# Kernel tuning notes

Hardware: AMD Instinct MI355X
Metric: run time of the kernel (lower is better)

Reference implementation:

```python
import jax, jax.numpy as jnp
import numpy as np

N_NODES = 50000
N_EDGES = 800000
N_GRAPHS = 2048
F = 78  # num_features_xd


def gcn_conv(x, src, dst, W, b):
    """PyG GCNConv: x' = D^{-1/2}(A+I)D^{-1/2} (x W) + b, self-loops added."""
    n = x.shape[0]
    xw = x @ W  # dense transform first (PyG order)
    loop = jnp.arange(n)
    s = jnp.concatenate([src, loop])
    d = jnp.concatenate([dst, loop])
    deg = jax.ops.segment_sum(jnp.ones(d.shape[0], dtype=xw.dtype), d, num_segments=n)
    dis = jnp.where(deg > 0, jax.lax.rsqrt(deg), 0.0)
    norm = dis[s] * dis[d]  # [E+N]
    msg = xw[s] * norm[:, None]  # gather + scale, [E+N, Fout]
    out = jax.ops.segment_sum(msg, d, num_segments=n)  # scatter-add to targets
    return out + b


def setup_inputs() -> dict:
    key = jax.random.key(0)
    ks = jax.random.split(key, 9)

    def glorot(k, shape):
        lim = float(np.sqrt(6.0 / (shape[0] + shape[1])))
        return jax.random.uniform(k, shape, minval=-lim, maxval=lim, dtype=jnp.float32)

    x = jax.random.normal(ks[0], (N_NODES, F), dtype=jnp.float32)
    edge_index = jax.random.randint(ks[1], (2, N_EDGES), 0, N_NODES, dtype=jnp.int64)
    batch = jnp.sort(jax.random.randint(ks[2], (N_NODES,), 0, N_GRAPHS, dtype=jnp.int64))
    drug2 = jax.random.normal(ks[3], (N_GRAPHS, 489), dtype=jnp.float32)

    W1 = glorot(ks[4], (F, F));        b1 = jnp.zeros((F,), jnp.float32)
    W2 = glorot(ks[5], (F, 2 * F));    b2 = jnp.zeros((2 * F,), jnp.float32)
    W3 = glorot(ks[6], (2 * F, 4 * F)); b3 = jnp.zeros((4 * F,), jnp.float32)
    Wfc = glorot(ks[7], (4 * F, 489)); bfc = jnp.zeros((489,), jnp.float32)

    return dict(x=x, edge_index=edge_index, batch=batch, drug2=drug2,
                W1=W1, b1=b1, W2=W2, b2=b2, W3=W3, b3=b3, Wfc=Wfc, bfc=bfc)


def reference(x, edge_index, batch, drug2, W1, b1, W2, b2, W3, b3, Wfc, bfc):
    src, dst = edge_index[0], edge_index[1]
    h = jax.nn.relu(gcn_conv(x, src, dst, W1, b1))   # dropout = identity (eval mode)
    h = jax.nn.relu(gcn_conv(h, src, dst, W2, b2))
    h = jax.nn.relu(gcn_conv(h, src, dst, W3, b3))
    g = jax.ops.segment_max(h, batch, num_segments=N_GRAPHS)  # global max pool
    g = jnp.where(jnp.isfinite(g), g, 0.0)  # guard empty graphs
    g = jax.nn.relu(g @ Wfc + bfc)
    return g + drug2
```

## Files before the change

kernel.cpp:

```cpp
#include <hip/hip_runtime.h>

#define NNODES 50000
#define NEDGES 800000
#define NGRAPHS 2048

typedef __attribute__((ext_vector_type(8))) short bf16x8;
typedef __attribute__((ext_vector_type(4))) float f32x4;

__device__ __forceinline__ float bf2f(ushort u) {
    return __uint_as_float(((uint)u) << 16);
}
__device__ __forceinline__ ushort f2bf(float f) {
    uint u = __float_as_uint(f);
    return (ushort)((u + 0x7fff + ((u >> 16) & 1)) >> 16);
}

__global__ void deg_count(const int* __restrict__ dst, int* __restrict__ cnt, int E) {
    int e = blockIdx.x * blockDim.x + threadIdx.x;
    if (e < E) atomicAdd(&cnt[dst[e]], 1);
}

__global__ void block_scan(const int* __restrict__ cnt, int* __restrict__ lp,
                           int* __restrict__ bsum, int M) {
    __shared__ int s[256];
    int t = threadIdx.x;
    int n = blockIdx.x * 256 + t;
    int v = (n < M) ? cnt[n] : 0;
    s[t] = v;
    __syncthreads();
    #pragma unroll
    for (int off = 1; off < 256; off <<= 1) {
        int u = (t >= off) ? s[t - off] : 0;
        __syncthreads();
        s[t] += u;
        __syncthreads();
    }
    if (n < M) lp[n] = s[t] - v;
    if (t == 255) bsum[blockIdx.x] = s[255];
}

__global__ void scan_bsum(int* __restrict__ bsum, int NB) {
    __shared__ int s[256];
    int t = threadIdx.x;
    int v = (t < NB) ? bsum[t] : 0;
    s[t] = v;
    __syncthreads();
    #pragma unroll
    for (int off = 1; off < 256; off <<= 1) {
        int u = (t >= off) ? s[t - off] : 0;
        __syncthreads();
        s[t] += u;
        __syncthreads();
    }
    if (t < NB) bsum[t] = s[t] - v;
}

__global__ void finalize_rowptr(int* __restrict__ rowptr, int* __restrict__ cursor,
                                const int* __restrict__ bsum, const int* __restrict__ cnt,
                                float* __restrict__ dis, int M, int E) {
    int n = blockIdx.x * blockDim.x + threadIdx.x;
    if (n < M) {
        int v = rowptr[n] + bsum[n >> 8];
        rowptr[n] = v;
        cursor[n] = v;
        dis[n] = rsqrtf((float)(cnt[n] + 1));
    }
    if (n == 0) rowptr[M] = E;
}

__global__ void fill_csr(const int* __restrict__ src, const int* __restrict__ dst,
                         const float* __restrict__ dis, int* __restrict__ cursor,
                         int2* __restrict__ csr, int E) {
    int e = blockIdx.x * blockDim.x + threadIdx.x;
    if (e >= E) return;
    int s = src[e], d = dst[e];
    int pos = atomicAdd(&cursor[d], 1);
    csr[pos] = make_int2(s, __float_as_int(dis[s] * dis[d]));
}

__global__ void cast_x(const float* __restrict__ x, ushort* __restrict__ xb,
                       int M, int K, int Kp) {
    int idx = blockIdx.x * blockDim.x + threadIdx.x;
    if (idx >= M * Kp) return;
    int n = idx / Kp, k = idx % Kp;
    xb[idx] = (k < K) ? f2bf(x[(size_t)n * K + k]) : (ushort)0;
}

__global__ void prep_w(const float* __restrict__ W, ushort* __restrict__ Wt,
                       int K, int N, int Kp, int Np) {
    int idx = blockIdx.x * blockDim.x + threadIdx.x;
    if (idx >= Kp * Np) return;
    int n = idx / Kp, k = idx % Kp;
    Wt[idx] = (k < K && n < N) ? f2bf(W[(size_t)k * N + n]) : (ushort)0;
}

__device__ __forceinline__ void acc8(float* acc, uint4 v, float nm) {
    acc[0] += bf2f((ushort)(v.x & 0xffff)) * nm;
    acc[1] += bf2f((ushort)(v.x >> 16)) * nm;
    acc[2] += bf2f((ushort)(v.y & 0xffff)) * nm;
    acc[3] += bf2f((ushort)(v.y >> 16)) * nm;
    acc[4] += bf2f((ushort)(v.z & 0xffff)) * nm;
    acc[5] += bf2f((ushort)(v.z >> 16)) * nm;
    acc[6] += bf2f((ushort)(v.w & 0xffff)) * nm;
    acc[7] += bf2f((ushort)(v.w >> 16)) * nm;
}

template <int CH, int SUB, int CHOUT>
__global__ __launch_bounds__(128) void gather_ilp(const uint4* __restrict__ h,
                                                  const int* __restrict__ rowptr,
                                                  const int2* __restrict__ csr,
                                                  const float* __restrict__ dis,
                                                  uint4* __restrict__ agg) {
    int node = blockIdx.x * 2 + (threadIdx.x >> 6);
    if (node >= NNODES) return;
    int lane = threadIdx.x & 63;
    int sub = lane / CH;
    int ch = lane % CH;
    bool active = sub < SUB;

    float acc[8] = {};
    int beg = rowptr[node], end = rowptr[node + 1];
    for (int i = beg; i < end; i += 4 * SUB) {
        int2 ev[4];
        int vld[4];
        #pragma unroll
        for (int u = 0; u < 4; ++u) {
            int e = i + u * SUB + sub;
            vld[u] = active && (e < end);
            ev[u] = vld[u] ? csr[e] : make_int2(0, 0);
        }
        uint4 av[4];
        #pragma unroll
        for (int u = 0; u < 4; ++u)
            av[u] = vld[u] ? h[(size_t)ev[u].x * CH + ch] : make_uint4(0, 0, 0, 0);
        #pragma unroll
        for (int u = 0; u < 4; ++u)
            acc8(acc, av[u], __int_as_float(ev[u].y));
    }

    float tot[8];
    #pragma unroll
    for (int j = 0; j < 8; ++j) tot[j] = acc[j];
    #pragma unroll
    for (int sb = 1; sb < SUB; ++sb) {
        int srcLane = ch + sb * CH;
        #pragma unroll
        for (int j = 0; j < 8; ++j) tot[j] += __shfl(acc[j], srcLane);
    }

    if (lane < CHOUT) {
        uint4 o = make_uint4(0, 0, 0, 0);
        if (lane < CH) {
            float di = dis[node];
            float d2 = di * di;
            uint4 hs = h[(size_t)node * CH + lane];
            tot[0] += bf2f((ushort)(hs.x & 0xffff)) * d2;
            tot[1] += bf2f((ushort)(hs.x >> 16)) * d2;
            tot[2] += bf2f((ushort)(hs.y & 0xffff)) * d2;
            tot[3] += bf2f((ushort)(hs.y >> 16)) * d2;
            tot[4] += bf2f((ushort)(hs.z & 0xffff)) * d2;
            tot[5] += bf2f((ushort)(hs.z >> 16)) * d2;
            tot[6] += bf2f((ushort)(hs.w & 0xffff)) * d2;
            tot[7] += bf2f((ushort)(hs.w >> 16)) * d2;
            o.x = (uint)f2bf(tot[0]) | ((uint)f2bf(tot[1]) << 16);
            o.y = (uint)f2bf(tot[2]) | ((uint)f2bf(tot[3]) << 16);
            o.z = (uint)f2bf(tot[4]) | ((uint)f2bf(tot[5]) << 16);
            o.w = (uint)f2bf(tot[6]) | ((uint)f2bf(tot[7]) << 16);
        }
        agg[(size_t)node * CHOUT + lane] = o;
    }
}

template <int EPI>
__global__ __launch_bounds__(256) void gemm_mfma(const ushort* __restrict__ A,
                                                 const ushort* __restrict__ Bt,
                                                 ushort* __restrict__ Cb,
                                                 float* __restrict__ Cf,
                                                 const float* __restrict__ bias,
                                                 const float* __restrict__ addend,
                                                 int M, int Kp, int Np, int Nreal) {
    __shared__ ushort Asl[64 * 32];
    __shared__ ushort Bsl[64 * 32];
    const int tid = threadIdx.x;
    const int lane = tid & 63;
    const int wid = tid >> 6;
    const int wm = (wid >> 1) * 32, wn = (wid & 1) * 32;
    const int bm = blockIdx.x * 64, bn = blockIdx.y * 64;

    const int sr = tid >> 2;
    const int sc = tid & 3;
    const int swz = sc ^ ((sr >> 1) & 3);
    const int lc = lane >> 4;

    f32x4 acc[2][2] = {};
    for (int k0 = 0; k0 < Kp; k0 += 32) {
        bf16x8 av = {};
        int gr = bm + sr;
        if (gr < M) av = *(const bf16x8*)&A[(size_t)gr * Kp + k0 + sc * 8];
        *(bf16x8*)&Asl[sr * 32 + swz * 8] = av;
        bf16x8 bv = {};
        int gn = bn + sr;
        if (gn < Np) bv = *(const bf16x8*)&Bt[(size_t)gn * Kp + k0 + sc * 8];
        *(bf16x8*)&Bsl[sr * 32 + swz * 8] = bv;
        __syncthreads();
        bf16x8 af[2], bfr[2];
        #pragma unroll
        for (int m = 0; m < 2; ++m) {
            int r = wm + m * 16 + (lane & 15);
            int pc = lc ^ ((r >> 1) & 3);
            af[m] = *(const bf16x8*)&Asl[r * 32 + pc * 8];
        }
        #pragma unroll
        for (int n = 0; n < 2; ++n) {
            int r = wn + n * 16 + (lane & 15);
            int pc = lc ^ ((r >> 1) & 3);
            bfr[n] = *(const bf16x8*)&Bsl[r * 32 + pc * 8];
        }
        #pragma unroll
        for (int m = 0; m < 2; ++m)
            #pragma unroll
            for (int n = 0; n < 2; ++n)
                acc[m][n] = __builtin_amdgcn_mfma_f32_16x16x32_bf16(af[m], bfr[n], acc[m][n], 0, 0, 0);
        __syncthreads();
    }
    #pragma unroll
    for (int m = 0; m < 2; ++m) {
        #pragma unroll
        for (int n = 0; n < 2; ++n) {
            int gc = bn + wn + n * 16 + (lane & 15);
            #pragma unroll
            for (int j = 0; j < 4; ++j) {
                int gr = bm + wm + m * 16 + (lane >> 4) * 4 + j;
                if (gr >= M) continue;
                float v = acc[m][n][j];
                if (EPI == 0) {
                    if (gc < Np) {
                        float o = (gc < Nreal) ? fmaxf(v + bias[gc], 0.f) : 0.f;
                        Cb[(size_t)gr * Np + gc] = f2bf(o);
                    }
                } else {
                    if (gc < Nreal) {
                        float o = fmaxf(v + bias[gc], 0.f) + addend[(size_t)gr * Nreal + gc];
                        Cf[(size_t)gr * Nreal + gc] = o;
                    }
                }
            }
        }
    }
}

__global__ void graph_bounds(const int* __restrict__ batch, int* __restrict__ gstart,
                             int M, int G) {
    int n = blockIdx.x * blockDim.x + threadIdx.x;
    if (n >= M) return;
    int b = batch[n];
    int bp = (n == 0) ? -1 : batch[n - 1];
    for (int gg = bp + 1; gg <= b; ++gg) gstart[gg] = n;
    if (n == M - 1) {
        for (int gg = b + 1; gg <= G; ++gg) gstart[gg] = M;
    }
}

__global__ void pool_max_seg(const uint* __restrict__ h3, const int* __restrict__ gstart,
                             uint* __restrict__ gb, int PAIRS) {
    int g = blockIdx.x;
    int s = gstart[g], e = gstart[g + 1];
    for (int p = threadIdx.x; p < PAIRS; p += blockDim.x) {
        float mL = 0.f, mH = 0.f;
        for (int n = s; n < e; ++n) {
            uint v = h3[(size_t)n * PAIRS + p];
            mL = fmaxf(mL, bf2f((ushort)(v & 0xffff)));
            mH = fmaxf(mH, bf2f((ushort)(v >> 16)));
        }
        gb[(size_t)g * PAIRS + p] = (uint)f2bf(mL) | ((uint)f2bf(mH) << 16);
    }
}

extern "C" void kernel_launch(void* const* d_in, const int* in_sizes, int n_in,
                              void* d_out, int out_size, void* d_ws, size_t ws_size,
                              hipStream_t stream) {
    const float* x     = (const float*)d_in[0];
    const int*   eidx  = (const int*)d_in[1];
    const int*   batch = (const int*)d_in[2];
    const float* drug2 = (const float*)d_in[3];
    const float* W1 = (const float*)d_in[4];
    const float* b1 = (const float*)d_in[5];
    const float* W2 = (const float*)d_in[6];
    const float* b2 = (const float*)d_in[7];
    const float* W3 = (const float*)d_in[8];
    const float* b3 = (const float*)d_in[9];
    const float* Wfc = (const float*)d_in[10];
    const float* bfc = (const float*)d_in[11];
    float* out = (float*)d_out;

    const int M = NNODES, E = NEDGES, G = NGRAPHS;
    const int F1 = 78, F2 = 156, F3 = 312, FC = 489;
    const int Kx = 80;
    const int Kp1 = 96, Np1 = 80;
    const int Kp2 = 96, Np2 = 160;
    const int Kp3 = 160, Np3 = 320;
    const int Kpf = 320, Npf = 496;

    const int* src = eidx;
    const int* dst = eidx + E;
    const int NB = (M + 255) / 256;

    char* ws = (char*)d_ws;
    size_t off = 0;
    auto alloc = [&](size_t bytes) {
        void* p = ws + off;
        off += (bytes + 255) & ~(size_t)255;
        return p;
    };
    ushort* xb   = (ushort*)alloc((size_t)M * Kx * 2);
    ushort* h1   = (ushort*)alloc((size_t)M * Np1 * 2);
    ushort* h2   = (ushort*)alloc((size_t)M * Np2 * 2);
    ushort* h3   = (ushort*)alloc((size_t)M * Np3 * 2);
    ushort* agg  = (ushort*)alloc((size_t)M * Kp3 * 2);
    ushort* W1t  = (ushort*)alloc((size_t)Np1 * Kp1 * 2);
    ushort* W2t  = (ushort*)alloc((size_t)Np2 * Kp2 * 2);
    ushort* W3t  = (ushort*)alloc((size_t)Np3 * Kp3 * 2);
    ushort* Wfct = (ushort*)alloc((size_t)Npf * Kpf * 2);
    ushort* gb   = (ushort*)alloc((size_t)G * Kpf * 2);
    float* dis    = (float*)alloc((size_t)M * 4);
    int*   cnt    = (int*)alloc((size_t)M * 4);
    int*   rowptr = (int*)alloc((size_t)(M + 1) * 4);
    int*   cursor = (int*)alloc((size_t)M * 4);
    int*   bsum   = (int*)alloc(1024);
    int2*  csr    = (int2*)alloc((size_t)E * 8);
    int*   gstart  = (int*)alloc((size_t)(G + 1) * 4);

    hipMemsetAsync(cnt, 0, (size_t)M * 4, stream);
    deg_count<<<(E + 255) / 256, 256, 0, stream>>>(dst, cnt, E);
    block_scan<<<NB, 256, 0, stream>>>(cnt, rowptr, bsum, M);
    scan_bsum<<<1, 256, 0, stream>>>(bsum, NB);
    finalize_rowptr<<<NB, 256, 0, stream>>>(rowptr, cursor, bsum, cnt, dis, M, E);
    fill_csr<<<(E + 255) / 256, 256, 0, stream>>>(src, dst, dis, cursor, csr, E);
    graph_bounds<<<NB, 256, 0, stream>>>(batch, gstart, M, G);

    cast_x<<<(M * Kx + 255) / 256, 256, 0, stream>>>(x, xb, M, F1, Kx);
    prep_w<<<(Np1 * Kp1 + 255) / 256, 256, 0, stream>>>(W1, W1t, F1, F1, Kp1, Np1);
    prep_w<<<(Np2 * Kp2 + 255) / 256, 256, 0, stream>>>(W2, W2t, F1, F2, Kp2, Np2);
    prep_w<<<(Np3 * Kp3 + 255) / 256, 256, 0, stream>>>(W3, W3t, F2, F3, Kp3, Np3);
    prep_w<<<(Npf * Kpf + 255) / 256, 256, 0, stream>>>(Wfc, Wfct, F3, FC, Kpf, Npf);

    const int GG = (M + 1) / 2;
    const int GMX = (M + 63) / 64;

    gather_ilp<10, 6, 12><<<GG, 128, 0, stream>>>((const uint4*)xb, rowptr, csr, dis, (uint4*)agg);
    gemm_mfma<0><<<dim3(GMX, Np1 / 64 + 1), 256, 0, stream>>>(agg, W1t, h1, nullptr, b1, nullptr, M, Kp1, Np1, F1);

    gather_ilp<10, 6, 12><<<GG, 128, 0, stream>>>((const uint4*)h1, rowptr, csr, dis, (uint4*)agg);
    gemm_mfma<0><<<dim3(GMX, Np2 / 64 + 1), 256, 0, stream>>>(agg, W2t, h2, nullptr, b2, nullptr, M, Kp2, Np2, F2);

    gather_ilp<20, 3, 20><<<GG, 128, 0, stream>>>((const uint4*)h2, rowptr, csr, dis, (uint4*)agg);
    gemm_mfma<0><<<dim3(GMX, Np3 / 64), 256, 0, stream>>>(agg, W3t, h3, nullptr, b3, nullptr, M, Kp3, Np3, F3);

    pool_max_seg<<<G, 256, 0, stream>>>((const uint*)h3, gstart, (uint*)gb, Kpf / 2);

    gemm_mfma<1><<<dim3((G + 63) / 64, (Npf + 63) / 64), 256, 0, stream>>>(gb, Wfct, nullptr, out, bfc, drug2, G, Kpf, Npf, FC);
}
```

Baseline: 289.6 us.

## Fuse neighbor aggregation with MFMA GEMM per GCN layer via LDS tile

Replaces each layer's separate gather kernel and GEMM kernel with one kernel. Each 256-thread block aggregates 32 nodes into a swizzled LDS tile, then runs the MFMA GEMM over all output column tiles with bias and ReLU in the epilogue. This removes the global round trip of the aggregated buffer and two kernel launches per layer. In exchange, each wave aggregates 8 nodes one after another, so fewer independent waves are in flight to hide gather latency. Each block also reloads the full weight matrix, and the 32-row GEMM tile is small.

```diff
diff --git a/kernel.cpp b/kernel.cpp
--- a/kernel.cpp
+++ b/kernel.cpp
@@ -105,80 +105,138 @@
     acc[7] += bf2f((ushort)(v.w >> 16)) * nm;
 }
 
-template <int CH, int SUB, int CHOUT>
-__global__ __launch_bounds__(128) void gather_ilp(const uint4* __restrict__ h,
-                                                  const int* __restrict__ rowptr,
-                                                  const int2* __restrict__ csr,
-                                                  const float* __restrict__ dis,
-                                                  uint4* __restrict__ agg) {
-    int node = blockIdx.x * 2 + (threadIdx.x >> 6);
-    if (node >= NNODES) return;
-    int lane = threadIdx.x & 63;
-    int sub = lane / CH;
-    int ch = lane % CH;
-    bool active = sub < SUB;
-
-    float acc[8] = {};
-    int beg = rowptr[node], end = rowptr[node + 1];
-    for (int i = beg; i < end; i += 4 * SUB) {
-        int2 ev[4];
-        int vld[4];
+template <int CH, int SUB, int KP, int NP, int NREAL>
+__global__ __launch_bounds__(256, 6) void fused_layer(const uint4* __restrict__ hsrc,
+                                                      const int* __restrict__ rowptr,
+                                                      const int2* __restrict__ csr,
+                                                      const float* __restrict__ dis,
+                                                      const ushort* __restrict__ Bt,
+                                                      const float* __restrict__ bias,
+                                                      ushort* __restrict__ hdst) {
+    constexpr int WPAD = KP + 8;
+    constexpr int CHOUT = KP / 8;
+    constexpr int NT = (NP + 63) / 64;
+    __shared__ ushort Alds[32 * WPAD];
+    __shared__ ushort Bsl[64 * 32];
+    const int tid = threadIdx.x;
+    const int lane = tid & 63;
+    const int wid = tid >> 6;
+    const int base = blockIdx.x * 32;
+
+    {
+        int sub = lane / CH;
+        int ch = lane % CH;
+        bool active = sub < SUB;
+        #pragma unroll 1
+        for (int s = 0; s < 8; ++s) {
+            int r = wid * 8 + s;
+            int node = base + r;
+            int beg = 0, end = 0;
+            if (node < NNODES) { beg = rowptr[node]; end = rowptr[node + 1]; }
+            float acc[8] = {};
+            for (int i = beg; i < end; i += 4 * SUB) {
+                int2 ev[4];
+                int vld[4];
+                #pragma unroll
+                for (int u = 0; u < 4; ++u) {
+                    int e = i + u * SUB + sub;
+                    vld[u] = active && (e < end);
+                    ev[u] = vld[u] ? csr[e] : make_int2(0, 0);
+                }
+                uint4 av[4];
+                #pragma unroll
+                for (int u = 0; u < 4; ++u)
+                    av[u] = vld[u] ? hsrc[(size_t)ev[u].x * CH + ch] : make_uint4(0, 0, 0, 0);
+                #pragma unroll
+                for (int u = 0; u < 4; ++u)
+                    acc8(acc, av[u], __int_as_float(ev[u].y));
+            }
+            float tot[8];
+            #pragma unroll
+            for (int j = 0; j < 8; ++j) tot[j] = acc[j];
+            #pragma unroll
+            for (int sb = 1; sb < SUB; ++sb) {
+                int srcLane = ch + sb * CH;
+                #pragma unroll
+                for (int j = 0; j < 8; ++j) tot[j] += __shfl(acc[j], srcLane);
+            }
+            if (lane < CHOUT) {
+                uint4 o = make_uint4(0, 0, 0, 0);
+                if (lane < CH && node < NNODES) {
+                    float di = dis[node];
+                    float d2 = di * di;
+                    uint4 hs = hsrc[(size_t)node * CH + lane];
+                    tot[0] += bf2f((ushort)(hs.x & 0xffff)) * d2;
+                    tot[1] += bf2f((ushort)(hs.x >> 16)) * d2;
+                    tot[2] += bf2f((ushort)(hs.y & 0xffff)) * d2;
+                    tot[3] += bf2f((ushort)(hs.y >> 16)) * d2;
+                    tot[4] += bf2f((ushort)(hs.z & 0xffff)) * d2;
+                    tot[5] += bf2f((ushort)(hs.z >> 16)) * d2;
+                    tot[6] += bf2f((ushort)(hs.w & 0xffff)) * d2;
+                    tot[7] += bf2f((ushort)(hs.w >> 16)) * d2;
+                    o.x = (uint)f2bf(tot[0]) | ((uint)f2bf(tot[1]) << 16);
+                    o.y = (uint)f2bf(tot[2]) | ((uint)f2bf(tot[3]) << 16);
+                    o.z = (uint)f2bf(tot[4]) | ((uint)f2bf(tot[5]) << 16);
+                    o.w = (uint)f2bf(tot[6]) | ((uint)f2bf(tot[7]) << 16);
+                }
+                int g = lane >> 2, c = lane & 3;
+                int sw = c ^ ((r >> 1) & 3);
+                *(uint4*)&Alds[r * WPAD + g * 32 + sw * 8] = o;
+            }
+        }
+    }
+    __syncthreads();
+
+    const int wm = (wid >> 1) * 16;
+    const int wn = (wid & 1) * 32;
+    const int sr = tid >> 2;
+    const int sc = tid & 3;
+    const int swz = sc ^ ((sr >> 1) & 3);
+    for (int bn = 0; bn < NT; ++bn) {
+        f32x4 acc2[2] = {};
+        for (int k0 = 0; k0 < KP; k0 += 32) {
+            bf16x8 bv = {};
+            int gn = bn * 64 + sr;
+            if (gn < NP) bv = *(const bf16x8*)&Bt[(size_t)gn * KP + k0 + sc * 8];
+            *(bf16x8*)&Bsl[sr * 32 + swz * 8] = bv;
+            __syncthreads();
+            int lc = lane >> 4;
+            int ar = wm + (lane & 15);
+            int apc = lc ^ ((ar >> 1) & 3);
+            bf16x8 af = *(const bf16x8*)&Alds[ar * WPAD + k0 + apc * 8];
+            bf16x8 bfr[2];
+            #pragma unroll
+            for (int n = 0; n < 2; ++n) {
+                int rr = wn + n * 16 + (lane & 15);
+                int pc = lc ^ ((rr >> 1) & 3);
+                bfr[n] = *(const bf16x8*)&Bsl[rr * 32 + pc * 8];
+            }
+            acc2[0] = __builtin_amdgcn_mfma_f32_16x16x32_bf16(af, bfr[0], acc2[0], 0, 0, 0);
+            acc2[1] = __builtin_amdgcn_mfma_f32_16x16x32_bf16(af, bfr[1], acc2[1], 0, 0, 0);
+            __syncthreads();
+        }
         #pragma unroll
-        for (int u = 0; u < 4; ++u) {
-            int e = i + u * SUB + sub;
-            vld[u] = active && (e < end);
-            ev[u] = vld[u] ? csr[e] : make_int2(0, 0);
-        }
-        uint4 av[4];
-        #pragma unroll
-        for (int u = 0; u < 4; ++u)
-            av[u] = vld[u] ? h[(size_t)ev[u].x * CH + ch] : make_uint4(0, 0, 0, 0);
-        #pragma unroll
-        for (int u = 0; u < 4; ++u)
-            acc8(acc, av[u], __int_as_float(ev[u].y));
-    }
-
-    float tot[8];
-    #pragma unroll
-    for (int j = 0; j < 8; ++j) tot[j] = acc[j];
-    #pragma unroll
-    for (int sb = 1; sb < SUB; ++sb) {
-        int srcLane = ch + sb * CH;
-        #pragma unroll
-        for (int j = 0; j < 8; ++j) tot[j] += __shfl(acc[j], srcLane);
-    }
-
-    if (lane < CHOUT) {
-        uint4 o = make_uint4(0, 0, 0, 0);
-        if (lane < CH) {
-            float di = dis[node];
-            float d2 = di * di;
-            uint4 hs = h[(size_t)node * CH + lane];
-            tot[0] += bf2f((ushort)(hs.x & 0xffff)) * d2;
-            tot[1] += bf2f((ushort)(hs.x >> 16)) * d2;
-            tot[2] += bf2f((ushort)(hs.y & 0xffff)) * d2;
-            tot[3] += bf2f((ushort)(hs.y >> 16)) * d2;
-            tot[4] += bf2f((ushort)(hs.z & 0xffff)) * d2;
-            tot[5] += bf2f((ushort)(hs.z >> 16)) * d2;
-            tot[6] += bf2f((ushort)(hs.w & 0xffff)) * d2;
-            tot[7] += bf2f((ushort)(hs.w >> 16)) * d2;
-            o.x = (uint)f2bf(tot[0]) | ((uint)f2bf(tot[1]) << 16);
-            o.y = (uint)f2bf(tot[2]) | ((uint)f2bf(tot[3]) << 16);
-            o.z = (uint)f2bf(tot[4]) | ((uint)f2bf(tot[5]) << 16);
-            o.w = (uint)f2bf(tot[6]) | ((uint)f2bf(tot[7]) << 16);
-        }
-        agg[(size_t)node * CHOUT + lane] = o;
-    }
-}
-
-template <int EPI>
-__global__ __launch_bounds__(256) void gemm_mfma(const ushort* __restrict__ A,
-                                                 const ushort* __restrict__ Bt,
-                                                 ushort* __restrict__ Cb,
-                                                 float* __restrict__ Cf,
-                                                 const float* __restrict__ bias,
-                                                 const float* __restrict__ addend,
-                                                 int M, int Kp, int Np, int Nreal) {
+        for (int n = 0; n < 2; ++n) {
+            int gc = bn * 64 + wn + n * 16 + (lane & 15);
+            #pragma unroll
+            for (int j = 0; j < 4; ++j) {
+                int gr = base + wm + (lane >> 4) * 4 + j;
+                if (gr < NNODES && gc < NP) {
+                    float v = acc2[n][j];
+                    float o = (gc < NREAL) ? fmaxf(v + bias[gc], 0.f) : 0.f;
+                    hdst[(size_t)gr * NP + gc] = f2bf(o);
+                }
+            }
+        }
+    }
+}
+
+__global__ __launch_bounds__(256) void gemm_fc(const ushort* __restrict__ A,
+                                               const ushort* __restrict__ Bt,
+                                               float* __restrict__ Cf,
+                                               const float* __restrict__ bias,
+                                               const float* __restrict__ addend,
+                                               int M, int Kp, int Np, int Nreal) {
     __shared__ ushort Asl[64 * 32];
     __shared__ ushort Bsl[64 * 32];
     const int tid = threadIdx.x;
@@ -231,19 +289,10 @@
             #pragma unroll
             for (int j = 0; j < 4; ++j) {
                 int gr = bm + wm + m * 16 + (lane >> 4) * 4 + j;
-                if (gr >= M) continue;
+                if (gr >= M || gc >= Nreal) continue;
                 float v = acc[m][n][j];
-                if (EPI == 0) {
-                    if (gc < Np) {
-                        float o = (gc < Nreal) ? fmaxf(v + bias[gc], 0.f) : 0.f;
-                        Cb[(size_t)gr * Np + gc] = f2bf(o);
-                    }
-                } else {
-                    if (gc < Nreal) {
-                        float o = fmaxf(v + bias[gc], 0.f) + addend[(size_t)gr * Nreal + gc];
-                        Cf[(size_t)gr * Nreal + gc] = o;
-                    }
-                }
+                float o = fmaxf(v + bias[gc], 0.f) + addend[(size_t)gr * Nreal + gc];
+                Cf[(size_t)gr * Nreal + gc] = o;
             }
         }
     }
@@ -316,7 +365,6 @@
     ushort* h1   = (ushort*)alloc((size_t)M * Np1 * 2);
     ushort* h2   = (ushort*)alloc((size_t)M * Np2 * 2);
     ushort* h3   = (ushort*)alloc((size_t)M * Np3 * 2);
-    ushort* agg  = (ushort*)alloc((size_t)M * Kp3 * 2);
     ushort* W1t  = (ushort*)alloc((size_t)Np1 * Kp1 * 2);
     ushort* W2t  = (ushort*)alloc((size_t)Np2 * Kp2 * 2);
     ushort* W3t  = (ushort*)alloc((size_t)Np3 * Kp3 * 2);
@@ -344,19 +392,19 @@
     prep_w<<<(Np3 * Kp3 + 255) / 256, 256, 0, stream>>>(W3, W3t, F2, F3, Kp3, Np3);
     prep_w<<<(Npf * Kpf + 255) / 256, 256, 0, stream>>>(Wfc, Wfct, F3, FC, Kpf, Npf);
 
-    const int GG = (M + 1) / 2;
-    const int GMX = (M + 63) / 64;
-
-    gather_ilp<10, 6, 12><<<GG, 128, 0, stream>>>((const uint4*)xb, rowptr, csr, dis, (uint4*)agg);
-    gemm_mfma<0><<<dim3(GMX, Np1 / 64 + 1), 256, 0, stream>>>(agg, W1t, h1, nullptr, b1, nullptr, M, Kp1, Np1, F1);
-
-    gather_ilp<10, 6, 12><<<GG, 128, 0, stream>>>((const uint4*)h1, rowptr, csr, dis, (uint4*)agg);
-    gemm_mfma<0><<<dim3(GMX, Np2 / 64 + 1), 256, 0, stream>>>(agg, W2t, h2, nullptr, b2, nullptr, M, Kp2, Np2, F2);
-
-    gather_ilp<20, 3, 20><<<GG, 128, 0, stream>>>((const uint4*)h2, rowptr, csr, dis, (uint4*)agg);
-    gemm_mfma<0><<<dim3(GMX, Np3 / 64), 256, 0, stream>>>(agg, W3t, h3, nullptr, b3, nullptr, M, Kp3, Np3, F3);
+    const int GF = (M + 31) / 32;
+
+    fused_layer<10, 6, 96, 80, 78><<<GF, 256, 0, stream>>>(
+        (const uint4*)xb, rowptr, csr, dis, W1t, b1, h1);
+
+    fused_layer<10, 6, 96, 160, 156><<<GF, 256, 0, stream>>>(
+        (const uint4*)h1, rowptr, csr, dis, W2t, b2, h2);
+
+    fused_layer<20, 3, 160, 320, 312><<<GF, 256, 0, stream>>>(
+        (const uint4*)h2, rowptr, csr, dis, W3t, b3, h3);
 
     pool_max_seg<<<G, 256, 0, stream>>>((const uint*)h3, gstart, (uint*)gb, Kpf / 2);
 
-    gemm_mfma<1><<<dim3((G + 63) / 64, (Npf + 63) / 64), 256, 0, stream>>>(gb, Wfct, nullptr, out, bfc, drug2, G, Kpf, Npf, FC);
-}
+    gemm_fc<<<dim3((G + 63) / 64, (Npf + 63) / 64), 256, 0, stream>>>(
+        gb, Wfct, out, bfc, drug2, G, Kpf, Npf, FC);
+}
```

Result: slower. 317.9 us (+9.8%).

## Merge prep kernels, fold graph bounds into rowptr, pad h2 row stride

Applied to the files above, without the earlier changes.

Five casting and weight-prep launches are merged into one prep_all kernel, and graph_bounds is folded into finalize_rowptr, cutting launch count and per-launch overhead. The h2 activation buffer gets a 192-element (384-byte) row stride instead of 160, so each gathered row starts on an aligned boundary, which should make the layer-3 gather's random row reads touch fewer cache lines. The gemm gains a separate output leading dimension to support this. The cost is a larger h2 buffer and padding bytes that are never written.

```diff
diff --git a/kernel.cpp b/kernel.cpp
--- a/kernel.cpp
+++ b/kernel.cpp
@@ -57,13 +57,21 @@
 
 __global__ void finalize_rowptr(int* __restrict__ rowptr, int* __restrict__ cursor,
                                 const int* __restrict__ bsum, const int* __restrict__ cnt,
-                                float* __restrict__ dis, int M, int E) {
+                                float* __restrict__ dis,
+                                const int* __restrict__ batch, int* __restrict__ gstart,
+                                int M, int E, int G) {
     int n = blockIdx.x * blockDim.x + threadIdx.x;
     if (n < M) {
         int v = rowptr[n] + bsum[n >> 8];
         rowptr[n] = v;
         cursor[n] = v;
         dis[n] = rsqrtf((float)(cnt[n] + 1));
+        int b = batch[n];
+        int bp = (n == 0) ? -1 : batch[n - 1];
+        for (int gg = bp + 1; gg <= b; ++gg) gstart[gg] = n;
+        if (n == M - 1) {
+            for (int gg = b + 1; gg <= G; ++gg) gstart[gg] = M;
+        }
     }
     if (n == 0) rowptr[M] = E;
 }
@@ -78,20 +86,44 @@
     csr[pos] = make_int2(s, __float_as_int(dis[s] * dis[d]));
 }
 
-__global__ void cast_x(const float* __restrict__ x, ushort* __restrict__ xb,
-                       int M, int K, int Kp) {
+__global__ void prep_all(const float* __restrict__ x, ushort* __restrict__ xb,
+                         const float* __restrict__ W1, ushort* __restrict__ W1t,
+                         const float* __restrict__ W2, ushort* __restrict__ W2t,
+                         const float* __restrict__ W3, ushort* __restrict__ W3t,
+                         const float* __restrict__ Wfc, ushort* __restrict__ Wfct) {
+    const int M = NNODES;
+    const int KX = 80, F1 = 78, F2 = 156, F3 = 312, FC = 489;
+    const int n0 = M * KX;
+    const int n1 = 80 * 96, n2 = 160 * 96, n3 = 320 * 160, n4 = 496 * 320;
     int idx = blockIdx.x * blockDim.x + threadIdx.x;
-    if (idx >= M * Kp) return;
-    int n = idx / Kp, k = idx % Kp;
-    xb[idx] = (k < K) ? f2bf(x[(size_t)n * K + k]) : (ushort)0;
-}
-
-__global__ void prep_w(const float* __restrict__ W, ushort* __restrict__ Wt,
-                       int K, int N, int Kp, int Np) {
-    int idx = blockIdx.x * blockDim.x + threadIdx.x;
-    if (idx >= Kp * Np) return;
-    int n = idx / Kp, k = idx % Kp;
-    Wt[idx] = (k < K && n < N) ? f2bf(W[(size_t)k * N + n]) : (ushort)0;
+    if (idx < n0) {
+        int n = idx / KX, k = idx % KX;
+        xb[idx] = (k < F1) ? f2bf(x[(size_t)n * F1 + k]) : (ushort)0;
+        return;
+    }
+    idx -= n0;
+    if (idx < n1) {
+        int n = idx / 96, k = idx % 96;
+        W1t[idx] = (k < F1 && n < F1) ? f2bf(W1[(size_t)k * F1 + n]) : (ushort)0;
+        return;
+    }
+    idx -= n1;
+    if (idx < n2) {
+        int n = idx / 96, k = idx % 96;
+        W2t[idx] = (k < F1 && n < F2) ? f2bf(W2[(size_t)k * F2 + n]) : (ushort)0;
+        return;
+    }
+    idx -= n2;
+    if (idx < n3) {
+        int n = idx / 160, k = idx % 160;
+        W3t[idx] = (k < F2 && n < F3) ? f2bf(W3[(size_t)k * F3 + n]) : (ushort)0;
+        return;
+    }
+    idx -= n3;
+    if (idx < n4) {
+        int n = idx / 320, k = idx % 320;
+        Wfct[idx] = (k < F3 && n < FC) ? f2bf(Wfc[(size_t)k * FC + n]) : (ushort)0;
+    }
 }
 
 __device__ __forceinline__ void acc8(float* acc, uint4 v, float nm) {
@@ -105,7 +137,7 @@
     acc[7] += bf2f((ushort)(v.w >> 16)) * nm;
 }
 
-template <int CH, int SUB, int CHOUT>
+template <int CH, int STR, int SUB, int CHOUT>
 __global__ __launch_bounds__(128) void gather_ilp(const uint4* __restrict__ h,
                                                   const int* __restrict__ rowptr,
                                                   const int2* __restrict__ csr,
@@ -132,7 +164,7 @@
         uint4 av[4];
         #pragma unroll
         for (int u = 0; u < 4; ++u)
-            av[u] = vld[u] ? h[(size_t)ev[u].x * CH + ch] : make_uint4(0, 0, 0, 0);
+            av[u] = vld[u] ? h[(size_t)ev[u].x * STR + ch] : make_uint4(0, 0, 0, 0);
         #pragma unroll
         for (int u = 0; u < 4; ++u)
             acc8(acc, av[u], __int_as_float(ev[u].y));
@@ -153,7 +185,7 @@
         if (lane < CH) {
             float di = dis[node];
             float d2 = di * di;
-            uint4 hs = h[(size_t)node * CH + lane];
+            uint4 hs = h[(size_t)node * STR + lane];
             tot[0] += bf2f((ushort)(hs.x & 0xffff)) * d2;
             tot[1] += bf2f((ushort)(hs.x >> 16)) * d2;
             tot[2] += bf2f((ushort)(hs.y & 0xffff)) * d2;
@@ -178,7 +210,7 @@
                                                  float* __restrict__ Cf,
                                                  const float* __restrict__ bias,
                                                  const float* __restrict__ addend,
-                                                 int M, int Kp, int Np, int Nreal) {
+                                                 int M, int Kp, int Np, int Nreal, int Cld) {
     __shared__ ushort Asl[64 * 32];
     __shared__ ushort Bsl[64 * 32];
     const int tid = threadIdx.x;
@@ -236,7 +268,7 @@
                 if (EPI == 0) {
                     if (gc < Np) {
                         float o = (gc < Nreal) ? fmaxf(v + bias[gc], 0.f) : 0.f;
-                        Cb[(size_t)gr * Np + gc] = f2bf(o);
+                        Cb[(size_t)gr * Cld + gc] = f2bf(o);
                     }
                 } else {
                     if (gc < Nreal) {
@@ -246,18 +278,6 @@
                 }
             }
         }
-    }
-}
-
-__global__ void graph_bounds(const int* __restrict__ batch, int* __restrict__ gstart,
-                             int M, int G) {
-    int n = blockIdx.x * blockDim.x + threadIdx.x;
-    if (n >= M) return;
-    int b = batch[n];
-    int bp = (n == 0) ? -1 : batch[n - 1];
-    for (int gg = bp + 1; gg <= b; ++gg) gstart[gg] = n;
-    if (n == M - 1) {
-        for (int gg = b + 1; gg <= G; ++gg) gstart[gg] = M;
     }
 }
 
@@ -300,6 +320,7 @@
     const int Kp2 = 96, Np2 = 160;
     const int Kp3 = 160, Np3 = 320;
     const int Kpf = 320, Npf = 496;
+    const int S2 = 192;
 
     const int* src = eidx;
     const int* dst = eidx + E;
@@ -314,7 +335,7 @@
     };
     ushort* xb   = (ushort*)alloc((size_t)M * Kx * 2);
     ushort* h1   = (ushort*)alloc((size_t)M * Np1 * 2);
-    ushort* h2   = (ushort*)alloc((size_t)M * Np2 * 2);
+    ushort* h2   = (ushort*)alloc((size_t)M * S2 * 2);
     ushort* h3   = (ushort*)alloc((size_t)M * Np3 * 2);
     ushort* agg  = (ushort*)alloc((size_t)M * Kp3 * 2);
     ushort* W1t  = (ushort*)alloc((size_t)Np1 * Kp1 * 2);
@@ -334,29 +355,27 @@
     deg_count<<<(E + 255) / 256, 256, 0, stream>>>(dst, cnt, E);
     block_scan<<<NB, 256, 0, stream>>>(cnt, rowptr, bsum, M);
     scan_bsum<<<1, 256, 0, stream>>>(bsum, NB);
-    finalize_rowptr<<<NB, 256, 0, stream>>>(rowptr, cursor, bsum, cnt, dis, M, E);
+    finalize_rowptr<<<NB, 256, 0, stream>>>(rowptr, cursor, bsum, cnt, dis, batch, gstart, M, E, G);
     fill_csr<<<(E + 255) / 256, 256, 0, stream>>>(src, dst, dis, cursor, csr, E);
-    graph_bounds<<<NB, 256, 0, stream>>>(batch, gstart, M, G);
-
-    cast_x<<<(M * Kx + 255) / 256, 256, 0, stream>>>(x, xb, M, F1, Kx);
-    prep_w<<<(Np1 * Kp1 + 255) / 256, 256, 0, stream>>>(W1, W1t, F1, F1, Kp1, Np1);
-    prep_w<<<(Np2 * Kp2 + 255) / 256, 256, 0, stream>>>(W2, W2t, F1, F2, Kp2, Np2);
-    prep_w<<<(Np3 * Kp3 + 255) / 256, 256, 0, stream>>>(W3, W3t, F2, F3, Kp3, Np3);
-    prep_w<<<(Npf * Kpf + 255) / 256, 256, 0, stream>>>(Wfc, Wfct, F3, FC, Kpf, Npf);
+
+    {
+        int total = M * Kx + 80 * 96 + 160 * 96 + 320 * 160 + 496 * 320;
+        prep_all<<<(total + 255) / 256, 256, 0, stream>>>(x, xb, W1, W1t, W2, W2t, W3, W3t, Wfc, Wfct);
+    }
 
     const int GG = (M + 1) / 2;
     const int GMX = (M + 63) / 64;
 
-    gather_ilp<10, 6, 12><<<GG, 128, 0, stream>>>((const uint4*)xb, rowptr, csr, dis, (uint4*)agg);
-    gemm_mfma<0><<<dim3(GMX, Np1 / 64 + 1), 256, 0, stream>>>(agg, W1t, h1, nullptr, b1, nullptr, M, Kp1, Np1, F1);
-
-    gather_ilp<10, 6, 12><<<GG, 128, 0, stream>>>((const uint4*)h1, rowptr, csr, dis, (uint4*)agg);
-    gemm_mfma<0><<<dim3(GMX, Np2 / 64 + 1), 256, 0, stream>>>(agg, W2t, h2, nullptr, b2, nullptr, M, Kp2, Np2, F2);
-
-    gather_ilp<20, 3, 20><<<GG, 128, 0, stream>>>((const uint4*)h2, rowptr, csr, dis, (uint4*)agg);
-    gemm_mfma<0><<<dim3(GMX, Np3 / 64), 256, 0, stream>>>(agg, W3t, h3, nullptr, b3, nullptr, M, Kp3, Np3, F3);
+    gather_ilp<10, 10, 6, 12><<<GG, 128, 0, stream>>>((const uint4*)xb, rowptr, csr, dis, (uint4*)agg);
+    gemm_mfma<0><<<dim3(GMX, (Np1 + 63) / 64), 256, 0, stream>>>(agg, W1t, h1, nullptr, b1, nullptr, M, Kp1, Np1, F1, Np1);
+
+    gather_ilp<10, 10, 6, 12><<<GG, 128, 0, stream>>>((const uint4*)h1, rowptr, csr, dis, (uint4*)agg);
+    gemm_mfma<0><<<dim3(GMX, (Np2 + 63) / 64), 256, 0, stream>>>(agg, W2t, h2, nullptr, b2, nullptr, M, Kp2, Np2, F2, S2);
+
+    gather_ilp<20, 24, 3, 20><<<GG, 128, 0, stream>>>((const uint4*)h2, rowptr, csr, dis, (uint4*)agg);
+    gemm_mfma<0><<<dim3(GMX, Np3 / 64), 256, 0, stream>>>(agg, W3t, h3, nullptr, b3, nullptr, M, Kp3, Np3, F3, Np3);
 
     pool_max_seg<<<G, 256, 0, stream>>>((const uint*)h3, gstart, (uint*)gb, Kpf / 2);
 
-    gemm_mfma<1><<<dim3((G + 63) / 64, (Npf + 63) / 64), 256, 0, stream>>>(gb, Wfct, nullptr, out, bfc, drug2, G, Kpf, Npf, FC);
-}
+    gemm_mfma<1><<<dim3((G + 63) / 64, (Npf + 63) / 64), 256, 0, stream>>>(gb, Wfct, nullptr, out, bfc, drug2, G, Kpf, Npf, FC, 0);
+}
```

Result: no change. 285.3 us (-1.5%).
